# Kernel tuning notes

Measured on AMD Instinct MI355X. Metric: run time of the kernel, lower is better.

The kernel has to match this reference:

```python
import jax, jax.numpy as jnp
import numpy as np

D_IN = 1024
D_OUT = 1024
N_HEADS = 16
HEAD_DIM = D_OUT // N_HEADS


def setup_inputs() -> dict:
    key = jax.random.key(0)
    ks = jax.random.split(key, 6)
    s = 0.02
    return {
        "X": jax.random.normal(ks[0], (4, 2048, D_IN), dtype=jnp.float32),
        "W_K": jax.random.normal(ks[1], (D_IN, D_OUT), dtype=jnp.float32) * s,
        "W_Q": jax.random.normal(ks[2], (D_IN, D_OUT), dtype=jnp.float32) * s,
        "W_V": jax.random.normal(ks[3], (D_IN, D_OUT), dtype=jnp.float32) * s,
        "W_out": jax.random.normal(ks[4], (D_OUT, D_OUT), dtype=jnp.float32) * s,
        "b_out": jax.random.normal(ks[5], (D_OUT,), dtype=jnp.float32) * s,
    }


def reference(X, W_K, W_Q, W_V, W_out, b_out):
    B, S, _ = X.shape
    # QKV projections (no bias, qkv_bias=False)
    Q = (X @ W_Q).reshape(B, S, N_HEADS, HEAD_DIM).transpose(0, 2, 1, 3)  # [B,H,S,Dh]
    K = (X @ W_K).reshape(B, S, N_HEADS, HEAD_DIM).transpose(0, 2, 1, 3)
    V = (X @ W_V).reshape(B, S, N_HEADS, HEAD_DIM).transpose(0, 2, 1, 3)
    # scores, causal mask, scale (mask-then-scale == scale-then-mask for -inf)
    scores = jnp.einsum("bhqd,bhkd->bhqk", Q, K) / jnp.sqrt(jnp.float32(HEAD_DIM))
    causal = jnp.tril(jnp.ones((S, S), dtype=bool))
    scores = jnp.where(causal, scores, -jnp.inf)
    W = jax.nn.softmax(scores, axis=-1)
    # dropout is identity in eval mode (deterministic reference)
    C = jnp.einsum("bhqk,bhkd->bhqd", W, V)  # [B,H,S,Dh]
    C = C.transpose(0, 2, 1, 3).reshape(B, S, D_OUT)
    return C @ W_out + b_out
```

## Files before the change

### kernel.cpp

```cpp
#include <hip/hip_runtime.h>


typedef float  f32x4  __attribute__((ext_vector_type(4)));
typedef float  f32x16 __attribute__((ext_vector_type(16)));
typedef __bf16 bf16x8 __attribute__((ext_vector_type(8)));
typedef unsigned int u32x4 __attribute__((ext_vector_type(4)));

#define DIM   1024
#define SEQ   2048
#define HDIM  64

static __device__ __forceinline__ unsigned short f2bf(float f) {
  unsigned int u = __builtin_bit_cast(unsigned int, f);
  u += 0x7fffu + ((u >> 16) & 1u);
  return (unsigned short)(u >> 16);
}

static __device__ __forceinline__ float exp2a(float x) {
#if __has_builtin(__builtin_amdgcn_exp2f)
  return __builtin_amdgcn_exp2f(x);
#else
  return exp2f(x);
#endif
}

static __device__ __forceinline__ void pswap(unsigned& a, unsigned& b) {
#if __has_builtin(__builtin_amdgcn_permlane32_swap)
  auto r = __builtin_amdgcn_permlane32_swap(a, b, false, false);
  a = r[0]; b = r[1];
#else
  asm volatile("v_permlane32_swap_b32 %0, %1" : "+v"(a), "+v"(b));
#endif
}

#define CVTPK(lo_, hi_) ({ unsigned r_;                                                 \
  asm("v_cvt_pk_bf16_f32 %0, %1, %2" : "=v"(r_) : "v"(lo_), "v"(hi_)); r_; })

#define GLDS16(g, l)                                                                    \
  __builtin_amdgcn_global_load_lds((__attribute__((address_space(1))) void*)(g),        \
                                   (__attribute__((address_space(3))) void*)(l), 16, 0, 0)

__global__ __launch_bounds__(256) void convert_x(const float4* __restrict__ X,
                                                 ushort4* __restrict__ Xb) {
  int i = blockIdx.x * 256 + threadIdx.x;
  float4 v = X[i];
  ushort4 o;
  o.x = f2bf(v.x); o.y = f2bf(v.y); o.z = f2bf(v.z); o.w = f2bf(v.w);
  Xb[i] = o;
}

__global__ __launch_bounds__(256) void transpose_w(const float* __restrict__ WQ,
                                                   const float* __restrict__ WK,
                                                   const float* __restrict__ WV,
                                                   const float* __restrict__ WO,
                                                   unsigned short* __restrict__ WtAll) {
  const int z = blockIdx.z;
  const float* W = (z == 0) ? WQ : (z == 1) ? WK : (z == 2) ? WV : WO;
  unsigned short* Wt = WtAll + (size_t)z * (DIM * DIM);
  __shared__ float tile[32][33];
  const int tx = threadIdx.x, ty = threadIdx.y;
  const int n0 = blockIdx.x * 32, k0 = blockIdx.y * 32;
#pragma unroll
  for (int r = 0; r < 4; ++r)
    tile[ty + 8 * r][tx] = W[(size_t)(k0 + ty + 8 * r) * DIM + n0 + tx];
  __syncthreads();
#pragma unroll
  for (int r = 0; r < 4; ++r)
    Wt[(size_t)(n0 + ty + 8 * r) * DIM + k0 + tx] = f2bf(tile[tx][ty + 8 * r]);
}

__global__ __launch_bounds__(256) void gemm_qkv(const unsigned short* __restrict__ Xb,
                                                const unsigned short* __restrict__ WtAll,
                                                unsigned short* __restrict__ Qb,
                                                unsigned short* __restrict__ Kh,
                                                unsigned short* __restrict__ Vb) {
  const int z = blockIdx.z;
  const unsigned short* Wt = WtAll + (size_t)z * (DIM * DIM);
  const int m0 = blockIdx.x * 128, n0 = blockIdx.y * 128;
  const int lane = threadIdx.x & 63, wave = threadIdx.x >> 6;
  const int wr = wave >> 1, wc = wave & 1;
  const int l15 = lane & 15, lg = lane >> 4;
  const int rowA = lane >> 2, colA = (lane & 3) * 8;
  const int sA = wave * 2;
  __shared__ __align__(16) unsigned short As[128 * 32], Bs[128 * 32];
  f32x4 acc[4][4] = {};

  for (int kt = 0; kt < DIM; kt += 32) {
    GLDS16(Xb + (size_t)(m0 + (sA + 0) * 16 + rowA) * DIM + kt + colA, &As[(sA + 0) * 512]);
    GLDS16(Xb + (size_t)(m0 + (sA + 1) * 16 + rowA) * DIM + kt + colA, &As[(sA + 1) * 512]);
    GLDS16(Wt + (size_t)(n0 + (sA + 0) * 16 + rowA) * DIM + kt + colA, &Bs[(sA + 0) * 512]);
    GLDS16(Wt + (size_t)(n0 + (sA + 1) * 16 + rowA) * DIM + kt + colA, &Bs[(sA + 1) * 512]);
    asm volatile("s_waitcnt vmcnt(0)" ::: "memory");
    __syncthreads();
    bf16x8 af[4], bfr[4];
#pragma unroll
    for (int mi = 0; mi < 4; ++mi)
      af[mi] = *(const bf16x8*)&As[(wr * 64 + mi * 16 + l15) * 32 + lg * 8];
#pragma unroll
    for (int ni = 0; ni < 4; ++ni)
      bfr[ni] = *(const bf16x8*)&Bs[(wc * 64 + ni * 16 + l15) * 32 + lg * 8];
#pragma unroll
    for (int mi = 0; mi < 4; ++mi)
#pragma unroll
      for (int ni = 0; ni < 4; ++ni)
        acc[mi][ni] = __builtin_amdgcn_mfma_f32_16x16x32_bf16(af[mi], bfr[ni], acc[mi][ni], 0, 0, 0);
    __syncthreads();
  }

  if (z == 0) {
    const float scale = (float)(0.125 * 1.4426950408889634);
#pragma unroll
    for (int mi = 0; mi < 4; ++mi)
#pragma unroll
      for (int ni = 0; ni < 4; ++ni) {
        const int n = n0 + wc * 64 + ni * 16 + l15;
        const int mb = m0 + wr * 64 + mi * 16 + lg * 4;
#pragma unroll
        for (int r = 0; r < 4; ++r)
          Qb[(size_t)(mb + r) * DIM + n] = f2bf(acc[mi][ni][r] * scale);
      }
  } else if (z == 1) {
#pragma unroll
    for (int mi = 0; mi < 4; ++mi)
#pragma unroll
      for (int ni = 0; ni < 4; ++ni) {
        const int n = n0 + wc * 64 + ni * 16 + l15;
        const int h = n >> 6, d = n & 63;
        const int mb = m0 + wr * 64 + mi * 16 + lg * 4;
        const int b = mb >> 11, s = mb & 2047;
        const size_t base = ((size_t)(b * 16 + h) * 2048 + s) * 64 + d;
#pragma unroll
        for (int r = 0; r < 4; ++r)
          Kh[base + (size_t)r * 64] = f2bf(acc[mi][ni][r]);
      }
  } else {
#pragma unroll
    for (int mi = 0; mi < 4; ++mi)
#pragma unroll
      for (int ni = 0; ni < 4; ++ni) {
        const int n = n0 + wc * 64 + ni * 16 + l15;
        const int h = n >> 6, d = n & 63;
        const int mb = m0 + wr * 64 + mi * 16 + lg * 4;
        const int b = mb >> 11, s = mb & 2047;
        const int t = s >> 6, si = s & 63;
        ushort4 v;
        v.x = f2bf(acc[mi][ni][0]); v.y = f2bf(acc[mi][ni][1]);
        v.z = f2bf(acc[mi][ni][2]); v.w = f2bf(acc[mi][ni][3]);
        *(ushort4*)&Vb[((((size_t)(b * 16 + h) * 32 + t) * 64 + d) * 64) + si] = v;
      }
  }
}

__global__ __launch_bounds__(256) void attn(const unsigned short* __restrict__ Qb,
                                            const unsigned short* __restrict__ Kh,
                                            const unsigned short* __restrict__ Vb,
                                            unsigned short* __restrict__ Cb) {
  const int bh = blockIdx.x;
  const int qt = (gridDim.y - 1) - blockIdx.y;
  const int b = bh >> 4;
  const int tid = threadIdx.x;
  const int lane = tid & 63, wave = tid >> 6;
  const int l31 = lane & 31, hi = lane >> 5;
  const int swz = (l31 & 7) << 4;
  const int q_base = qt * 128 + wave * 32;
  const int q = q_base + l31;

  __shared__ __align__(16) char LDS[2][16384];

  int soff0, soff1;
  {
    const int L0 = wave * 2048 + lane * 16;
    const int r0 = L0 >> 7;
    soff0 = r0 * 128 + ((L0 & 127) ^ ((r0 & 7) << 4));
    const int L1 = L0 + 1024;
    const int r1 = L1 >> 7;
    soff1 = r1 * 128 + ((L1 & 127) ^ ((r1 & 7) << 4));
  }
  const char* Kt0 = (const char*)Kh + ((size_t)bh * 2048) * 128;
  const char* Vt0 = (const char*)Vb + ((size_t)bh * 32) * 8192;

  const unsigned short* Qp = Qb + (size_t)(b * SEQ + q) * DIM + (bh & 15) * HDIM + hi * 8;
  bf16x8 qf[4];
#pragma unroll
  for (int ks = 0; ks < 4; ++ks) qf[ks] = *(const bf16x8*)(Qp + ks * 16);

  float m_r = -INFINITY, l_r = 0.f;
  f32x16 o0 = {}, o1 = {};

  const int n_tiles = 2 * qt + 2;
  int cur = 0;

  {
    char* lK = &LDS[0][wave * 2048];
    char* lV = &LDS[0][8192 + wave * 2048];
    GLDS16(Kt0 + soff0, lK); GLDS16(Kt0 + soff1, lK + 1024);
    GLDS16(Vt0 + soff0, lV); GLDS16(Vt0 + soff1, lV + 1024);
  }
  __syncthreads();

  for (int t = 0; t < n_tiles; ++t) {
    const int kv0 = t << 6;
    if (t + 1 < n_tiles) {
      const char* kb = Kt0 + (size_t)(t + 1) * 8192;
      const char* vb = Vt0 + (size_t)(t + 1) * 8192;
      char* lK = &LDS[cur ^ 1][wave * 2048];
      char* lV = &LDS[cur ^ 1][8192 + wave * 2048];
      GLDS16(kb + soff0, lK); GLDS16(kb + soff1, lK + 1024);
      GLDS16(vb + soff0, lV); GLDS16(vb + soff1, lV + 1024);
    }

    if (kv0 <= q_base + 31) {
      const char* Lb = &LDS[cur][0];
      f32x16 st0 = {}, st1 = {};
      __builtin_amdgcn_s_setprio(1);
#pragma unroll
      for (int ks = 0; ks < 4; ++ks) {
        const char* a = Lb + l31 * 128 + ((ks * 32 + hi * 16) ^ swz);
        bf16x8 kf0 = *(const bf16x8*)(a);
        bf16x8 kf1 = *(const bf16x8*)(a + 4096);
        st0 = __builtin_amdgcn_mfma_f32_32x32x16_bf16(kf0, qf[ks], st0, 0, 0, 0);
        st1 = __builtin_amdgcn_mfma_f32_32x32x16_bf16(kf1, qf[ks], st1, 0, 0, 0);
      }
      __builtin_amdgcn_s_setprio(0);

      if (kv0 + 63 > q_base) {
        const int qm = q - kv0 - 4 * hi;
#pragma unroll
        for (int r = 0; r < 16; ++r) {
          const int c = (r & 3) + 8 * (r >> 2);
          if (c > qm)      st0[r] = -INFINITY;
          if (c + 32 > qm) st1[r] = -INFINITY;
        }
      }

      float tmax = st0[0];
#pragma unroll
      for (int r = 1; r < 16; ++r) tmax = fmaxf(tmax, st0[r]);
#pragma unroll
      for (int r = 0; r < 16; ++r) tmax = fmaxf(tmax, st1[r]);
      tmax = fmaxf(tmax, __shfl_xor(tmax, 32));

      if (__any(!(tmax <= m_r + 8.0f))) {
        const float mn = fmaxf(m_r, tmax);
        const float al = exp2a(m_r - mn);
        m_r = mn;
        l_r *= al;
        o0 *= al;
        o1 *= al;
      }

#pragma unroll
      for (int r = 0; r < 16; ++r) st0[r] = exp2a(st0[r] - m_r);
#pragma unroll
      for (int r = 0; r < 16; ++r) st1[r] = exp2a(st1[r] - m_r);
      float ps = 0.f;
#pragma unroll
      for (int r = 0; r < 16; ++r) ps += st0[r] + st1[r];
      ps += __shfl_xor(ps, 32);
      l_r += ps;

      u32x4 pf[4];
      {
        unsigned a, bb;
        a = CVTPK(st0[0], st0[1]);   bb = CVTPK(st0[4], st0[5]);   pswap(a, bb); pf[0][0] = a; pf[0][2] = bb;
        a = CVTPK(st0[2], st0[3]);   bb = CVTPK(st0[6], st0[7]);   pswap(a, bb); pf[0][1] = a; pf[0][3] = bb;
        a = CVTPK(st0[8], st0[9]);   bb = CVTPK(st0[12], st0[13]); pswap(a, bb); pf[1][0] = a; pf[1][2] = bb;
        a = CVTPK(st0[10], st0[11]); bb = CVTPK(st0[14], st0[15]); pswap(a, bb); pf[1][1] = a; pf[1][3] = bb;
        a = CVTPK(st1[0], st1[1]);   bb = CVTPK(st1[4], st1[5]);   pswap(a, bb); pf[2][0] = a; pf[2][2] = bb;
        a = CVTPK(st1[2], st1[3]);   bb = CVTPK(st1[6], st1[7]);   pswap(a, bb); pf[2][1] = a; pf[2][3] = bb;
        a = CVTPK(st1[8], st1[9]);   bb = CVTPK(st1[12], st1[13]); pswap(a, bb); pf[3][0] = a; pf[3][2] = bb;
        a = CVTPK(st1[10], st1[11]); bb = CVTPK(st1[14], st1[15]); pswap(a, bb); pf[3][1] = a; pf[3][3] = bb;
      }

      __builtin_amdgcn_s_setprio(1);
#pragma unroll
      for (int ks = 0; ks < 4; ++ks) {
        const char* a = Lb + 8192 + l31 * 128 + ((ks * 32 + hi * 16) ^ swz);
        bf16x8 v0 = *(const bf16x8*)(a);
        bf16x8 v1 = *(const bf16x8*)(a + 4096);
        bf16x8 pb = __builtin_bit_cast(bf16x8, pf[ks]);
        o0 = __builtin_amdgcn_mfma_f32_32x32x16_bf16(v0, pb, o0, 0, 0, 0);
        o1 = __builtin_amdgcn_mfma_f32_32x32x16_bf16(v1, pb, o1, 0, 0, 0);
      }
      __builtin_amdgcn_s_setprio(0);
    }

    __syncthreads();
    cur ^= 1;
  }

  const float rl = 1.0f / l_r;
  unsigned short* Co = Cb + (size_t)(b * SEQ + q) * DIM + (bh & 15) * HDIM;
#pragma unroll
  for (int j = 0; j < 4; ++j) {
    ushort4 w0, w1;
    w0.x = f2bf(o0[4 * j + 0] * rl); w0.y = f2bf(o0[4 * j + 1] * rl);
    w0.z = f2bf(o0[4 * j + 2] * rl); w0.w = f2bf(o0[4 * j + 3] * rl);
    w1.x = f2bf(o1[4 * j + 0] * rl); w1.y = f2bf(o1[4 * j + 1] * rl);
    w1.z = f2bf(o1[4 * j + 2] * rl); w1.w = f2bf(o1[4 * j + 3] * rl);
    *(ushort4*)(Co + 8 * j + 4 * hi) = w0;
    *(ushort4*)(Co + 32 + 8 * j + 4 * hi) = w1;
  }
}

__global__ __launch_bounds__(256) void gemm_out(const unsigned short* __restrict__ Cb,
                                                const unsigned short* __restrict__ WtO,
                                                const float* __restrict__ bias,
                                                float* __restrict__ out) {
  const int m0 = blockIdx.x * 128, n0 = blockIdx.y * 128;
  const int lane = threadIdx.x & 63, wave = threadIdx.x >> 6;
  const int wr = wave >> 1, wc = wave & 1;
  const int l15 = lane & 15, lg = lane >> 4;
  const int rowA = lane >> 2, colA = (lane & 3) * 8;
  const int sA = wave * 2;
  __shared__ __align__(16) unsigned short As[128 * 32], Bs[128 * 32];
  f32x4 acc[4][4] = {};

  for (int kt = 0; kt < DIM; kt += 32) {
    GLDS16(Cb  + (size_t)(m0 + (sA + 0) * 16 + rowA) * DIM + kt + colA, &As[(sA + 0) * 512]);
    GLDS16(Cb  + (size_t)(m0 + (sA + 1) * 16 + rowA) * DIM + kt + colA, &As[(sA + 1) * 512]);
    GLDS16(WtO + (size_t)(n0 + (sA + 0) * 16 + rowA) * DIM + kt + colA, &Bs[(sA + 0) * 512]);
    GLDS16(WtO + (size_t)(n0 + (sA + 1) * 16 + rowA) * DIM + kt + colA, &Bs[(sA + 1) * 512]);
    asm volatile("s_waitcnt vmcnt(0)" ::: "memory");
    __syncthreads();
    bf16x8 af[4], bfr[4];
#pragma unroll
    for (int mi = 0; mi < 4; ++mi)
      af[mi] = *(const bf16x8*)&As[(wr * 64 + mi * 16 + l15) * 32 + lg * 8];
#pragma unroll
    for (int ni = 0; ni < 4; ++ni)
      bfr[ni] = *(const bf16x8*)&Bs[(wc * 64 + ni * 16 + l15) * 32 + lg * 8];
#pragma unroll
    for (int mi = 0; mi < 4; ++mi)
#pragma unroll
      for (int ni = 0; ni < 4; ++ni)
        acc[mi][ni] = __builtin_amdgcn_mfma_f32_16x16x32_bf16(af[mi], bfr[ni], acc[mi][ni], 0, 0, 0);
    __syncthreads();
  }

#pragma unroll
  for (int ni = 0; ni < 4; ++ni) {
    const int n = n0 + wc * 64 + ni * 16 + l15;
    const float bv = bias[n];
#pragma unroll
    for (int mi = 0; mi < 4; ++mi) {
      const int mb = m0 + wr * 64 + mi * 16 + lg * 4;
#pragma unroll
      for (int r = 0; r < 4; ++r)
        out[(size_t)(mb + r) * DIM + n] = acc[mi][ni][r] + bv;
    }
  }
}

extern "C" void kernel_launch(void* const* d_in, const int* in_sizes, int n_in,
                              void* d_out, int out_size, void* d_ws, size_t ws_size,
                              hipStream_t stream) {
  const float* X  = (const float*)d_in[0];
  const float* WK = (const float*)d_in[1];
  const float* WQ = (const float*)d_in[2];
  const float* WV = (const float*)d_in[3];
  const float* WO = (const float*)d_in[4];
  const float* bo = (const float*)d_in[5];
  float* out = (float*)d_out;

  char* ws = (char*)d_ws;
  unsigned short* Xb    = (unsigned short*)(ws);
  unsigned short* WtAll = (unsigned short*)(ws + (16u << 20));
  unsigned short* Qb    = (unsigned short*)(ws + (24u << 20));
  unsigned short* Kh    = (unsigned short*)(ws + (40u << 20));
  unsigned short* Vb    = (unsigned short*)(ws + (56u << 20));
  unsigned short* Cb    = Xb;

  convert_x<<<8192, 256, 0, stream>>>((const float4*)X, (ushort4*)Xb);
  transpose_w<<<dim3(32, 32, 4), dim3(32, 8), 0, stream>>>(WQ, WK, WV, WO, WtAll);
  gemm_qkv<<<dim3(64, 8, 3), 256, 0, stream>>>(Xb, WtAll, Qb, Kh, Vb);
  attn<<<dim3(64, 16), 256, 0, stream>>>(Qb, Kh, Vb, Cb);
  gemm_out<<<dim3(64, 8), 256, 0, stream>>>(Cb, WtAll + 3u * 1048576u, bo, out);
}
```

Baseline: 261.7 us.

## Double-buffer LDS in projection GEMMs and vectorize epilogue stores via swapped MFMA operands

Both the QKV and output projection GEMMs now ping-pong between two LDS buffers, so the next K-tile's global-to-LDS loads are issued before the MFMAs on the current tile, and one barrier per iteration is dropped. MFMA A/B operands are swapped for the Q, K and output GEMMs, which transposes the accumulator layout so each lane holds four consecutive columns. That lets the epilogues write ushort4/float4 vectors and load the bias as float4 instead of issuing scalar strided stores. The explicit vmcnt(0) wait was removed, so correctness relies on the compiler inserting waits for the LDS-DMA loads before each barrier. LDS use per block doubles.

```diff
diff --git a/kernel.cpp b/kernel.cpp
--- a/kernel.cpp
+++ b/kernel.cpp
@@ -1,5 +1,4 @@
 #include <hip/hip_runtime.h>
-
 
 typedef float  f32x4  __attribute__((ext_vector_type(4)));
 typedef float  f32x16 __attribute__((ext_vector_type(16)));
@@ -82,29 +81,43 @@
   const int l15 = lane & 15, lg = lane >> 4;
   const int rowA = lane >> 2, colA = (lane & 3) * 8;
   const int sA = wave * 2;
-  __shared__ __align__(16) unsigned short As[128 * 32], Bs[128 * 32];
+  __shared__ __align__(16) unsigned short As[2][128 * 32], Bs[2][128 * 32];
   f32x4 acc[4][4] = {};
 
+  auto STAGE = [&](int buf, int kt) {
+    GLDS16(Xb + (size_t)(m0 + (sA + 0) * 16 + rowA) * DIM + kt + colA, &As[buf][(sA + 0) * 512]);
+    GLDS16(Xb + (size_t)(m0 + (sA + 1) * 16 + rowA) * DIM + kt + colA, &As[buf][(sA + 1) * 512]);
+    GLDS16(Wt + (size_t)(n0 + (sA + 0) * 16 + rowA) * DIM + kt + colA, &Bs[buf][(sA + 0) * 512]);
+    GLDS16(Wt + (size_t)(n0 + (sA + 1) * 16 + rowA) * DIM + kt + colA, &Bs[buf][(sA + 1) * 512]);
+  };
+
+  STAGE(0, 0);
+  __syncthreads();
+  int cur = 0;
   for (int kt = 0; kt < DIM; kt += 32) {
-    GLDS16(Xb + (size_t)(m0 + (sA + 0) * 16 + rowA) * DIM + kt + colA, &As[(sA + 0) * 512]);
-    GLDS16(Xb + (size_t)(m0 + (sA + 1) * 16 + rowA) * DIM + kt + colA, &As[(sA + 1) * 512]);
-    GLDS16(Wt + (size_t)(n0 + (sA + 0) * 16 + rowA) * DIM + kt + colA, &Bs[(sA + 0) * 512]);
-    GLDS16(Wt + (size_t)(n0 + (sA + 1) * 16 + rowA) * DIM + kt + colA, &Bs[(sA + 1) * 512]);
-    asm volatile("s_waitcnt vmcnt(0)" ::: "memory");
+    if (kt + 32 < DIM) STAGE(cur ^ 1, kt + 32);
+    bf16x8 af[4], bfr[4];
+#pragma unroll
+    for (int mi = 0; mi < 4; ++mi)
+      af[mi] = *(const bf16x8*)&As[cur][(wr * 64 + mi * 16 + l15) * 32 + lg * 8];
+#pragma unroll
+    for (int ni = 0; ni < 4; ++ni)
+      bfr[ni] = *(const bf16x8*)&Bs[cur][(wc * 64 + ni * 16 + l15) * 32 + lg * 8];
+    if (z < 2) {
+#pragma unroll
+      for (int mi = 0; mi < 4; ++mi)
+#pragma unroll
+        for (int ni = 0; ni < 4; ++ni)
+          acc[mi][ni] = __builtin_amdgcn_mfma_f32_16x16x32_bf16(bfr[ni], af[mi], acc[mi][ni], 0, 0, 0);
+    } else {
+#pragma unroll
+      for (int mi = 0; mi < 4; ++mi)
+#pragma unroll
+        for (int ni = 0; ni < 4; ++ni)
+          acc[mi][ni] = __builtin_amdgcn_mfma_f32_16x16x32_bf16(af[mi], bfr[ni], acc[mi][ni], 0, 0, 0);
+    }
     __syncthreads();
-    bf16x8 af[4], bfr[4];
-#pragma unroll
-    for (int mi = 0; mi < 4; ++mi)
-      af[mi] = *(const bf16x8*)&As[(wr * 64 + mi * 16 + l15) * 32 + lg * 8];
-#pragma unroll
-    for (int ni = 0; ni < 4; ++ni)
-      bfr[ni] = *(const bf16x8*)&Bs[(wc * 64 + ni * 16 + l15) * 32 + lg * 8];
-#pragma unroll
-    for (int mi = 0; mi < 4; ++mi)
-#pragma unroll
-      for (int ni = 0; ni < 4; ++ni)
-        acc[mi][ni] = __builtin_amdgcn_mfma_f32_16x16x32_bf16(af[mi], bfr[ni], acc[mi][ni], 0, 0, 0);
-    __syncthreads();
+    cur ^= 1;
   }
 
   if (z == 0) {
@@ -113,25 +126,26 @@
     for (int mi = 0; mi < 4; ++mi)
 #pragma unroll
       for (int ni = 0; ni < 4; ++ni) {
-        const int n = n0 + wc * 64 + ni * 16 + l15;
-        const int mb = m0 + wr * 64 + mi * 16 + lg * 4;
-#pragma unroll
-        for (int r = 0; r < 4; ++r)
-          Qb[(size_t)(mb + r) * DIM + n] = f2bf(acc[mi][ni][r] * scale);
+        const int s = m0 + wr * 64 + mi * 16 + l15;
+        const int nb = n0 + wc * 64 + ni * 16 + lg * 4;
+        ushort4 v;
+        v.x = f2bf(acc[mi][ni][0] * scale); v.y = f2bf(acc[mi][ni][1] * scale);
+        v.z = f2bf(acc[mi][ni][2] * scale); v.w = f2bf(acc[mi][ni][3] * scale);
+        *(ushort4*)&Qb[(size_t)s * DIM + nb] = v;
       }
   } else if (z == 1) {
 #pragma unroll
     for (int mi = 0; mi < 4; ++mi)
 #pragma unroll
       for (int ni = 0; ni < 4; ++ni) {
-        const int n = n0 + wc * 64 + ni * 16 + l15;
-        const int h = n >> 6, d = n & 63;
-        const int mb = m0 + wr * 64 + mi * 16 + lg * 4;
-        const int b = mb >> 11, s = mb & 2047;
-        const size_t base = ((size_t)(b * 16 + h) * 2048 + s) * 64 + d;
-#pragma unroll
-        for (int r = 0; r < 4; ++r)
-          Kh[base + (size_t)r * 64] = f2bf(acc[mi][ni][r]);
+        const int s = m0 + wr * 64 + mi * 16 + l15;
+        const int b = s >> 11, sl = s & 2047;
+        const int nb = n0 + wc * 64 + ni * 16 + lg * 4;
+        const int h = nb >> 6, d = nb & 63;
+        ushort4 v;
+        v.x = f2bf(acc[mi][ni][0]); v.y = f2bf(acc[mi][ni][1]);
+        v.z = f2bf(acc[mi][ni][2]); v.w = f2bf(acc[mi][ni][3]);
+        *(ushort4*)&Kh[((size_t)(b * 16 + h) * 2048 + sl) * 64 + d] = v;
       }
   } else {
 #pragma unroll
@@ -313,43 +327,49 @@
   const int l15 = lane & 15, lg = lane >> 4;
   const int rowA = lane >> 2, colA = (lane & 3) * 8;
   const int sA = wave * 2;
-  __shared__ __align__(16) unsigned short As[128 * 32], Bs[128 * 32];
+  __shared__ __align__(16) unsigned short As[2][128 * 32], Bs[2][128 * 32];
   f32x4 acc[4][4] = {};
 
+  auto STAGE = [&](int buf, int kt) {
+    GLDS16(Cb  + (size_t)(m0 + (sA + 0) * 16 + rowA) * DIM + kt + colA, &As[buf][(sA + 0) * 512]);
+    GLDS16(Cb  + (size_t)(m0 + (sA + 1) * 16 + rowA) * DIM + kt + colA, &As[buf][(sA + 1) * 512]);
+    GLDS16(WtO + (size_t)(n0 + (sA + 0) * 16 + rowA) * DIM + kt + colA, &Bs[buf][(sA + 0) * 512]);
+    GLDS16(WtO + (size_t)(n0 + (sA + 1) * 16 + rowA) * DIM + kt + colA, &Bs[buf][(sA + 1) * 512]);
+  };
+
+  STAGE(0, 0);
+  __syncthreads();
+  int cur = 0;
   for (int kt = 0; kt < DIM; kt += 32) {
-    GLDS16(Cb  + (size_t)(m0 + (sA + 0) * 16 + rowA) * DIM + kt + colA, &As[(sA + 0) * 512]);
-    GLDS16(Cb  + (size_t)(m0 + (sA + 1) * 16 + rowA) * DIM + kt + colA, &As[(sA + 1) * 512]);
-    GLDS16(WtO + (size_t)(n0 + (sA + 0) * 16 + rowA) * DIM + kt + colA, &Bs[(sA + 0) * 512]);
-    GLDS16(WtO + (size_t)(n0 + (sA + 1) * 16 + rowA) * DIM + kt + colA, &Bs[(sA + 1) * 512]);
-    asm volatile("s_waitcnt vmcnt(0)" ::: "memory");
+    if (kt + 32 < DIM) STAGE(cur ^ 1, kt + 32);
+    bf16x8 af[4], bfr[4];
+#pragma unroll
+    for (int mi = 0; mi < 4; ++mi)
+      af[mi] = *(const bf16x8*)&As[cur][(wr * 64 + mi * 16 + l15) * 32 + lg * 8];
+#pragma unroll
+    for (int ni = 0; ni < 4; ++ni)
+      bfr[ni] = *(const bf16x8*)&Bs[cur][(wc * 64 + ni * 16 + l15) * 32 + lg * 8];
+#pragma unroll
+    for (int mi = 0; mi < 4; ++mi)
+#pragma unroll
+      for (int ni = 0; ni < 4; ++ni)
+        acc[mi][ni] = __builtin_amdgcn_mfma_f32_16x16x32_bf16(bfr[ni], af[mi], acc[mi][ni], 0, 0, 0);
     __syncthreads();
-    bf16x8 af[4], bfr[4];
-#pragma unroll
-    for (int mi = 0; mi < 4; ++mi)
-      af[mi] = *(const bf16x8*)&As[(wr * 64 + mi * 16 + l15) * 32 + lg * 8];
-#pragma unroll
-    for (int ni = 0; ni < 4; ++ni)
-      bfr[ni] = *(const bf16x8*)&Bs[(wc * 64 + ni * 16 + l15) * 32 + lg * 8];
-#pragma unroll
-    for (int mi = 0; mi < 4; ++mi)
-#pragma unroll
-      for (int ni = 0; ni < 4; ++ni)
-        acc[mi][ni] = __builtin_amdgcn_mfma_f32_16x16x32_bf16(af[mi], bfr[ni], acc[mi][ni], 0, 0, 0);
-    __syncthreads();
-  }
-
-#pragma unroll
-  for (int ni = 0; ni < 4; ++ni) {
-    const int n = n0 + wc * 64 + ni * 16 + l15;
-    const float bv = bias[n];
-#pragma unroll
-    for (int mi = 0; mi < 4; ++mi) {
-      const int mb = m0 + wr * 64 + mi * 16 + lg * 4;
-#pragma unroll
-      for (int r = 0; r < 4; ++r)
-        out[(size_t)(mb + r) * DIM + n] = acc[mi][ni][r] + bv;
+    cur ^= 1;
+  }
+
+#pragma unroll
+  for (int mi = 0; mi < 4; ++mi)
+#pragma unroll
+    for (int ni = 0; ni < 4; ++ni) {
+      const int s = m0 + wr * 64 + mi * 16 + l15;
+      const int nb = n0 + wc * 64 + ni * 16 + lg * 4;
+      const float4 bv = *(const float4*)&bias[nb];
+      float4 o;
+      o.x = acc[mi][ni][0] + bv.x; o.y = acc[mi][ni][1] + bv.y;
+      o.z = acc[mi][ni][2] + bv.z; o.w = acc[mi][ni][3] + bv.w;
+      *(float4*)&out[(size_t)s * DIM + nb] = o;
     }
-  }
 }
 
 extern "C" void kernel_launch(void* const* d_in, const int* in_sizes, int n_in,
```

Measured after the change: 264.3 us. No clear change (+1.0%).
